# Performance work log

Measured on AMD Instinct MI355X. Metric: run time of the kernel, lower is better.

The kernel has to match this reference:

```python
import jax, jax.numpy as jnp
import numpy as np

N = 16384      # occupied voxels after upsample
M = 16384      # target (ground-truth) voxels
C = 64         # input feature channels
CU = 64        # upsampled feature channels
B = 4          # batch size (samples in sparse batch)
S = 64         # voxel grid span per axis
TARGET_POINTS_NUM = 8192   # points_num_list entry (kthvalue k)
DIST_UPPER_BOUND2 = 4.0    # dist_upper_bound ** 2


def _coord_key(c):
    # unique int64 key per (batch, x, y, z); all coords in [0, S)
    c = c.astype(jnp.int64)
    return ((c[:, 0] * S + c[:, 1]) * S + c[:, 2]) * S + c[:, 3]


def setup_inputs() -> dict:
    key = jax.random.key(0)
    k1, k2, k3, k4, k5, k6, k7 = jax.random.split(key, 7)
    fea = jax.random.normal(k1, (N, C), jnp.float32)
    coords = jnp.concatenate(
        [jax.random.randint(k2, (N, 1), 0, B, jnp.int32),
         jax.random.randint(k3, (N, 3), 0, S, jnp.int32)], axis=1)
    target_coords = jnp.concatenate(
        [jax.random.randint(k4, (M, 1), 0, B, jnp.int32),
         jax.random.randint(k5, (M, 3), 0, S, jnp.int32)], axis=1)
    W_up = jax.random.normal(k6, (C, CU), jnp.float32) / np.sqrt(C).astype(np.float32)
    W_cls = jax.random.normal(k7, (CU, 1), jnp.float32) / np.sqrt(CU).astype(np.float32)
    return {"fea": fea, "W_up": W_up, "W_cls": W_cls,
            "coords": coords, "target_coords": target_coords}


def reference(fea, W_up, W_cls, coords, target_coords):
    # upsample_block + classify_block (dense cores of the Minkowski blocks)
    fea_up = jax.nn.relu(fea @ W_up)              # [N, CU]
    pred = fea_up @ W_cls                          # [N, 1]
    p = pred[:, 0]

    # ---- keep mask ('Dist' loss: keep the TARGET_POINTS_NUM smallest) ----
    # torch.kthvalue(pred.F, k, dim=0): k-th smallest value
    thres = jnp.sort(p)[TARGET_POINTS_NUM - 1]
    keep = p <= thres                              # N > target_points_num branch

    # ---- get_target: keep_target via coordinate match (kernel_size=1 map) ----
    fk = _coord_key(coords)
    tk = jnp.sort(_coord_key(target_coords))
    idx = jnp.clip(jnp.searchsorted(tk, fk), 0, M - 1)
    keep_target = tk[idx] == fk                    # [N] bool

    # ---- get_target: per-sample K=1 KNN squared distances ----
    pc = coords[:, 1:].astype(jnp.float32)         # [N, 3]
    tc = target_coords[:, 1:].astype(jnp.float32)  # [M, 3]
    # |a-b|^2 = |a|^2 + |b|^2 - 2 a.b  (avoids [N,M,3] intermediate)
    d2 = (jnp.sum(pc * pc, -1)[:, None] + jnp.sum(tc * tc, -1)[None, :]
          - 2.0 * (pc @ tc.T))                     # [N, M]
    same_sample = coords[:, 0:1] == target_coords[None, :, 0]  # [N, M]
    d2 = jnp.where(same_sample, d2, jnp.inf)
    dists = jnp.maximum(jnp.min(d2, axis=1), 0.0)  # [N]

    # bound / ignore handling of loss_target
    pred_mask = p > DIST_UPPER_BOUND2
    target_mask = dists > DIST_UPPER_BOUND2
    loss_target = jnp.where(~pred_mask & target_mask, DIST_UPPER_BOUND2, dists)
    loss_target = jnp.where(pred_mask & target_mask, p, loss_target)

    keep = keep | keep_target
    # pruning: represented as masking (static shapes under jit)
    fea_pruned = fea_up * keep[:, None].astype(fea_up.dtype)
    return pred, fea_pruned, keep, keep_target, loss_target
```

## Files before the change

kernel.cpp:

```cpp
#include <hip/hip_runtime.h>
#include <math.h>

#define N_PTS 16384
#define M_TGT 16384
#define TPN 8192
#define DUB2 4.0f
#define BMASK_WORDS (4*64*64*64/32)
#define SCAT_NB 16

__device__ __forceinline__ unsigned int mono_key(float f) {
    unsigned int u = __float_as_uint(f);
    return (u & 0x80000000u) ? ~u : (u | 0x80000000u);
}

__device__ const signed char NOFF4[33][4] = {
    {0,0,0,0},
    {1,0,0,1},{-1,0,0,1},{0,1,0,1},{0,-1,0,1},{0,0,1,1},{0,0,-1,1},
    {1,1,0,2},{1,-1,0,2},{-1,1,0,2},{-1,-1,0,2},{1,0,1,2},{1,0,-1,2},{-1,0,1,2},{-1,0,-1,2},
    {0,1,1,2},{0,1,-1,2},{0,-1,1,2},{0,-1,-1,2},
    {1,1,1,3},{1,1,-1,3},{1,-1,1,3},{1,-1,-1,3},{-1,1,1,3},{-1,1,-1,3},{-1,-1,1,3},{-1,-1,-1,3},
    {2,0,0,4},{-2,0,0,4},{0,2,0,4},{0,-2,0,4},{0,0,2,4},{0,0,-2,4}
};

__device__ __forceinline__ void scan_locate256(const unsigned int* h256,
        unsigned int r, unsigned int* sh_b, unsigned int* sh_r, int tid) {
    const int lane = tid & 63;
    if ((tid >> 6) == 0) {
        uint4 h = ((const uint4*)h256)[lane];
        unsigned int ss = h.x + h.y + h.z + h.w;
        unsigned int inc = ss;
        for (int d = 1; d < 64; d <<= 1) {
            unsigned int t = __shfl_up(inc, d);
            if (lane >= d) inc += t;
        }
        unsigned int exc = inc - ss;
        bool has = (r >= exc && r < exc + ss);
        unsigned long long m = __ballot(has);
        if (m != 0ull && lane == __ffsll(m) - 1) {
            unsigned int rr = r - exc;
            if (rr < h.x)                   { *sh_b = lane*4u;    *sh_r = rr; }
            else if (rr < h.x+h.y)          { *sh_b = lane*4u+1u; *sh_r = rr-h.x; }
            else if (rr < h.x+h.y+h.z)      { *sh_b = lane*4u+2u; *sh_r = rr-h.x-h.y; }
            else                            { *sh_b = lane*4u+3u; *sh_r = rr-h.x-h.y-h.z; }
        }
    }
}

__global__ __launch_bounds__(256) void k_gemm(const float* __restrict__ fea,
        const float* __restrict__ Wup, const float* __restrict__ Wcls,
        float* __restrict__ out_pred, float* __restrict__ out_fea,
        unsigned int* __restrict__ bmask, unsigned int* __restrict__ hist16,
        unsigned int* __restrict__ phist) {
    __shared__ float Ws[64 * 64];
    __shared__ float fs[16 * 68];
    const int tid = threadIdx.x;
    const int r0 = blockIdx.x * 16;

    if (tid < 32) bmask[blockIdx.x * 32 + tid] = 0u;
    else if (tid < 96) hist16[blockIdx.x * 64 + tid - 32] = 0u;
    else if (tid < 100) phist[blockIdx.x * 4 + tid - 96] = 0u;

    for (int t = tid; t < 1024; t += 256)
        ((float4*)Ws)[t] = ((const float4*)Wup)[t];
    {
        float4 v = ((const float4*)(fea + r0 * 64))[tid];
        int r = tid >> 4, c = (tid & 15) * 4;
        fs[r*68 + c + 0] = v.x; fs[r*68 + c + 1] = v.y;
        fs[r*68 + c + 2] = v.z; fs[r*68 + c + 3] = v.w;
    }
    __syncthreads();

    const int cg = tid & 15;
    const int r  = tid >> 4;
    float a0 = 0.f, a1 = 0.f, a2 = 0.f, a3 = 0.f;
    const float* fr = fs + r * 68;
    #pragma unroll
    for (int k = 0; k < 64; ++k) {
        float f = fr[k];
        float4 w = *(const float4*)&Ws[k * 64 + cg * 4];
        a0 = fmaf(f, w.x, a0); a1 = fmaf(f, w.y, a1);
        a2 = fmaf(f, w.z, a2); a3 = fmaf(f, w.w, a3);
    }
    a0 = fmaxf(a0, 0.f); a1 = fmaxf(a1, 0.f);
    a2 = fmaxf(a2, 0.f); a3 = fmaxf(a3, 0.f);
    const int row = r0 + r;
    *(float4*)&out_fea[row * 64 + cg * 4] = make_float4(a0, a1, a2, a3);

    float4 wc = *(const float4*)&Wcls[cg * 4];
    float s = a0*wc.x + a1*wc.y + a2*wc.z + a3*wc.w;
    for (int off = 1; off < 16; off <<= 1) s += __shfl_xor(s, off, 16);
    if (cg == 0) out_pred[row] = s;
}

__global__ __launch_bounds__(256) void k_scat(const float* __restrict__ pred,
        const int* __restrict__ tc, unsigned int* __restrict__ bmask,
        unsigned int* __restrict__ phist, unsigned int* __restrict__ hist16) {
    __shared__ unsigned int whist[4][256];
    const int tid = threadIdx.x;
    const int blk = blockIdx.x;
    const int id = blk * 256 + tid;

    for (int t = tid; t < 4 * 256; t += 256) ((unsigned int*)whist)[t] = 0u;

    int4 c = *(const int4*)&tc[id * 4];
    int key = ((c.x * 64 + c.y) * 64 + c.z) * 64 + c.w;
    atomicOr(&bmask[key >> 5], 1u << (key & 31));

    __syncthreads();
    unsigned int u = mono_key(pred[id]);
    atomicAdd(&whist[tid >> 6][u >> 24], 1u);
    atomicAdd(&hist16[u >> 16], 1u);
    __syncthreads();
    {
        unsigned int s = whist[0][tid] + whist[1][tid] + whist[2][tid] + whist[3][tid];
        if (s) atomicAdd(&phist[(blk >> 2) * 256 + tid], s);
    }
}

__global__ __launch_bounds__(1024) void k_final(const int* __restrict__ coords,
        const unsigned int* __restrict__ bmask, const unsigned int* __restrict__ phist,
        const unsigned int* __restrict__ hist16,
        const float* __restrict__ out_pred, float* __restrict__ out_fea,
        float* __restrict__ out_keep, float* __restrict__ out_kt,
        float* __restrict__ out_loss) {
    __shared__ unsigned int hA[256];
    __shared__ unsigned int list[1024];
    __shared__ unsigned int sh_b, sh_r, sh_cnt;
    __shared__ float kscale[64];
    const int tid = threadIdx.x;
    const int r0 = blockIdx.x * 64;

    if (tid < 256) {
        unsigned int s = 0u;
        #pragma unroll
        for (int b = 0; b < SCAT_NB; ++b) s += phist[b * 256 + tid];
        hA[tid] = s;
    }
    if (tid == 0) sh_cnt = 0u;
    __syncthreads();
    scan_locate256(hA, TPN - 1, &sh_b, &sh_r, tid);
    __syncthreads();
    const unsigned int b0 = sh_b;
    const unsigned int rank1 = sh_r;

    if (tid < 256) hA[tid] = hist16[b0 * 256 + tid];
    __syncthreads();
    scan_locate256(hA, rank1, &sh_b, &sh_r, tid);
    __syncthreads();
    const unsigned int bin16 = (b0 << 8) | sh_b;
    const unsigned int rank2 = sh_r;

    for (int i = tid; i < N_PTS / 4; i += 1024) {
        float4 v = ((const float4*)out_pred)[i];
        unsigned int u0 = mono_key(v.x), u1 = mono_key(v.y);
        unsigned int u2 = mono_key(v.z), u3 = mono_key(v.w);
        if ((u0 >> 16) == bin16) { unsigned int p = atomicAdd(&sh_cnt, 1u); if (p < 1024u) list[p] = u0 & 0xFFFFu; }
        if ((u1 >> 16) == bin16) { unsigned int p = atomicAdd(&sh_cnt, 1u); if (p < 1024u) list[p] = u1 & 0xFFFFu; }
        if ((u2 >> 16) == bin16) { unsigned int p = atomicAdd(&sh_cnt, 1u); if (p < 1024u) list[p] = u2 & 0xFFFFu; }
        if ((u3 >> 16) == bin16) { unsigned int p = atomicAdd(&sh_cnt, 1u); if (p < 1024u) list[p] = u3 & 0xFFFFu; }
    }
    __syncthreads();
    const unsigned int cnt = sh_cnt;
    unsigned int b2, b3;

    if (cnt <= 1024u) {
        if (tid < 256) hA[tid] = 0u;
        __syncthreads();
        if (tid < (int)cnt) atomicAdd(&hA[list[tid] >> 8], 1u);
        __syncthreads();
        scan_locate256(hA, rank2, &sh_b, &sh_r, tid);
        __syncthreads();
        b2 = sh_b;
        unsigned int rank3 = sh_r;
        if (tid < 256) hA[tid] = 0u;
        __syncthreads();
        if (tid < (int)cnt) { unsigned int e = list[tid]; if ((e >> 8) == b2) atomicAdd(&hA[e & 255u], 1u); }
        __syncthreads();
        scan_locate256(hA, rank3, &sh_b, &sh_r, tid);
        __syncthreads();
        b3 = sh_b;
    } else {
        if (tid < 256) hA[tid] = 0u;
        __syncthreads();
        for (int i = tid; i < N_PTS / 4; i += 1024) {
            float4 v = ((const float4*)out_pred)[i];
            unsigned int u0 = mono_key(v.x), u1 = mono_key(v.y);
            unsigned int u2 = mono_key(v.z), u3 = mono_key(v.w);
            if ((u0 >> 16) == bin16) atomicAdd(&hA[(u0 >> 8) & 255u], 1u);
            if ((u1 >> 16) == bin16) atomicAdd(&hA[(u1 >> 8) & 255u], 1u);
            if ((u2 >> 16) == bin16) atomicAdd(&hA[(u2 >> 8) & 255u], 1u);
            if ((u3 >> 16) == bin16) atomicAdd(&hA[(u3 >> 8) & 255u], 1u);
        }
        __syncthreads();
        scan_locate256(hA, rank2, &sh_b, &sh_r, tid);
        __syncthreads();
        b2 = sh_b;
        unsigned int rank3 = sh_r;
        unsigned int pfx24 = (bin16 << 8) | b2;
        if (tid < 256) hA[tid] = 0u;
        __syncthreads();
        for (int i = tid; i < N_PTS / 4; i += 1024) {
            float4 v = ((const float4*)out_pred)[i];
            unsigned int u0 = mono_key(v.x), u1 = mono_key(v.y);
            unsigned int u2 = mono_key(v.z), u3 = mono_key(v.w);
            if ((u0 >> 8) == pfx24) atomicAdd(&hA[u0 & 255u], 1u);
            if ((u1 >> 8) == pfx24) atomicAdd(&hA[u1 & 255u], 1u);
            if ((u2 >> 8) == pfx24) atomicAdd(&hA[u2 & 255u], 1u);
            if ((u3 >> 8) == pfx24) atomicAdd(&hA[u3 & 255u], 1u);
        }
        __syncthreads();
        scan_locate256(hA, rank3, &sh_b, &sh_r, tid);
        __syncthreads();
        b3 = sh_b;
    }
    const unsigned int uth = (bin16 << 16) | (b2 << 8) | b3;
    const float thres = (uth & 0x80000000u) ? __uint_as_float(uth ^ 0x80000000u)
                                            : __uint_as_float(~uth);

    {
        const int row = tid >> 4;
        const int sub = tid & 15;
        const int i = r0 + row;
        float p = out_pred[i];
        int4 c = *(const int4*)&coords[i * 4];
        const int b = c.x, x = c.y, y = c.z, z = c.w;
        int key0 = ((b * 64 + x) * 64 + y) * 64 + z;
        bool kt = (bmask[key0 >> 5] >> (key0 & 31)) & 1u;
        float dists;
        if (kt) {
            dists = 0.f;
        } else {
            float best = 5.f;
            #pragma unroll
            for (int q = 0; q < 2; ++q) {
                int t = 1 + sub + q * 16;
                int ox = x + NOFF4[t][0], oy = y + NOFF4[t][1], oz = z + NOFF4[t][2];
                if (((unsigned)ox | (unsigned)oy | (unsigned)oz) < 64u) {
                    int key = ((b * 64 + ox) * 64 + oy) * 64 + oz;
                    if ((bmask[key >> 5] >> (key & 31)) & 1u)
                        best = fminf(best, (float)NOFF4[t][3]);
                }
            }
            for (int d = 1; d < 16; d <<= 1)
                best = fminf(best, __shfl_xor(best, d, 16));
            dists = best;
        }
        if (sub == 0) {
            bool keep0 = (p <= thres);
            bool pm = (p > DUB2), tm = (dists > DUB2);
            float loss = (pm && tm) ? p : ((!pm && tm) ? DUB2 : dists);
            bool kf = keep0 || kt;
            out_keep[i] = kf ? 1.f : 0.f;
            out_kt[i]  = kt ? 1.f : 0.f;
            out_loss[i] = loss;
            kscale[row] = kf ? 1.f : 0.f;
        }
    }
    __syncthreads();
    {
        float4* fbase = (float4*)(out_fea + r0 * 64);
        int v = tid;
        if (kscale[v >> 4] == 0.f)
            fbase[v] = make_float4(0.f, 0.f, 0.f, 0.f);
    }
}

extern "C" void kernel_launch(void* const* d_in, const int* in_sizes, int n_in,
                              void* d_out, int out_size, void* d_ws, size_t ws_size,
                              hipStream_t stream) {
    const float* fea     = (const float*)d_in[0];
    const float* Wup     = (const float*)d_in[1];
    const float* Wcls    = (const float*)d_in[2];
    const int*   coords  = (const int*)d_in[3];
    const int*   tcoords = (const int*)d_in[4];

    float* out      = (float*)d_out;
    float* out_pred = out;
    float* out_fea  = out + N_PTS;
    float* out_keep = out + N_PTS + N_PTS * 64;
    float* out_kt   = out_keep + N_PTS;
    float* out_loss = out_kt + N_PTS;

    char* ws = (char*)d_ws;
    unsigned int* bmask  = (unsigned int*)(ws + 64);
    unsigned int* hist16 = (unsigned int*)(ws + 131136);
    unsigned int* phist  = (unsigned int*)(ws + 393280);

    k_gemm <<<N_PTS / 16, 256, 0, stream>>>(fea, Wup, Wcls, out_pred, out_fea,
                                            bmask, hist16, phist);
    k_scat <<<64, 256, 0, stream>>>(out_pred, tcoords, bmask, phist, hist16);
    k_final<<<N_PTS / 64, 1024, 0, stream>>>(coords, bmask, phist, hist16,
                                             out_pred, out_fea, out_keep, out_kt, out_loss);
}
```

Before: 25.62 us.

## Fuse scatter and histogram into GEMM kernel, add separate zeroing kernel

The separate scatter kernel is removed. Target-coordinate bitmask marking and the pred radix histograms now happen inside the GEMM kernel, using global atomics directly on one 256-bin histogram instead of per-block partials. Workspace zeroing moves to a new small kernel launched first, so the launch count stays at three. This trades the scatter pass's extra read of pred for global atomic contention on hist16 and phist from every row.

```diff
diff --git a/kernel.cpp b/kernel.cpp
--- a/kernel.cpp
+++ b/kernel.cpp
@@ -5,8 +5,7 @@
 #define M_TGT 16384
 #define TPN 8192
 #define DUB2 4.0f
-#define BMASK_WORDS (4*64*64*64/32)
-#define SCAT_NB 16
+#define ZWORDS 98560
 
 __device__ __forceinline__ unsigned int mono_key(float f) {
     unsigned int u = __float_as_uint(f);
@@ -46,8 +45,14 @@
     }
 }
 
+__global__ __launch_bounds__(256) void k_zero(unsigned int* __restrict__ z) {
+    int i = blockIdx.x * 256 + threadIdx.x;
+    if (i < ZWORDS) z[i] = 0u;
+}
+
 __global__ __launch_bounds__(256) void k_gemm(const float* __restrict__ fea,
         const float* __restrict__ Wup, const float* __restrict__ Wcls,
+        const int* __restrict__ tcoords,
         float* __restrict__ out_pred, float* __restrict__ out_fea,
         unsigned int* __restrict__ bmask, unsigned int* __restrict__ hist16,
         unsigned int* __restrict__ phist) {
@@ -56,9 +61,11 @@
     const int tid = threadIdx.x;
     const int r0 = blockIdx.x * 16;
 
-    if (tid < 32) bmask[blockIdx.x * 32 + tid] = 0u;
-    else if (tid < 96) hist16[blockIdx.x * 64 + tid - 32] = 0u;
-    else if (tid < 100) phist[blockIdx.x * 4 + tid - 96] = 0u;
+    if (tid < 16) {
+        int4 c = *(const int4*)&tcoords[(blockIdx.x * 16 + tid) * 4];
+        int key = ((c.x * 64 + c.y) * 64 + c.z) * 64 + c.w;
+        atomicOr(&bmask[key >> 5], 1u << (key & 31));
+    }
 
     for (int t = tid; t < 1024; t += 256)
         ((float4*)Ws)[t] = ((const float4*)Wup)[t];
@@ -89,31 +96,11 @@
     float4 wc = *(const float4*)&Wcls[cg * 4];
     float s = a0*wc.x + a1*wc.y + a2*wc.z + a3*wc.w;
     for (int off = 1; off < 16; off <<= 1) s += __shfl_xor(s, off, 16);
-    if (cg == 0) out_pred[row] = s;
-}
-
-__global__ __launch_bounds__(256) void k_scat(const float* __restrict__ pred,
-        const int* __restrict__ tc, unsigned int* __restrict__ bmask,
-        unsigned int* __restrict__ phist, unsigned int* __restrict__ hist16) {
-    __shared__ unsigned int whist[4][256];
-    const int tid = threadIdx.x;
-    const int blk = blockIdx.x;
-    const int id = blk * 256 + tid;
-
-    for (int t = tid; t < 4 * 256; t += 256) ((unsigned int*)whist)[t] = 0u;
-
-    int4 c = *(const int4*)&tc[id * 4];
-    int key = ((c.x * 64 + c.y) * 64 + c.z) * 64 + c.w;
-    atomicOr(&bmask[key >> 5], 1u << (key & 31));
-
-    __syncthreads();
-    unsigned int u = mono_key(pred[id]);
-    atomicAdd(&whist[tid >> 6][u >> 24], 1u);
-    atomicAdd(&hist16[u >> 16], 1u);
-    __syncthreads();
-    {
-        unsigned int s = whist[0][tid] + whist[1][tid] + whist[2][tid] + whist[3][tid];
-        if (s) atomicAdd(&phist[(blk >> 2) * 256 + tid], s);
+    if (cg == 0) {
+        out_pred[row] = s;
+        unsigned int u = mono_key(s);
+        atomicAdd(&hist16[u >> 16], 1u);
+        atomicAdd(&phist[u >> 24], 1u);
     }
 }
 
@@ -130,12 +117,7 @@
     const int tid = threadIdx.x;
     const int r0 = blockIdx.x * 64;
 
-    if (tid < 256) {
-        unsigned int s = 0u;
-        #pragma unroll
-        for (int b = 0; b < SCAT_NB; ++b) s += phist[b * 256 + tid];
-        hA[tid] = s;
-    }
+    if (tid < 256) hA[tid] = phist[tid];
     if (tid == 0) sh_cnt = 0u;
     __syncthreads();
     scan_locate256(hA, TPN - 1, &sh_b, &sh_r, tid);
@@ -282,13 +264,14 @@
     float* out_loss = out_kt + N_PTS;
 
     char* ws = (char*)d_ws;
+    unsigned int* zbase  = (unsigned int*)(ws + 64);
     unsigned int* bmask  = (unsigned int*)(ws + 64);
     unsigned int* hist16 = (unsigned int*)(ws + 131136);
     unsigned int* phist  = (unsigned int*)(ws + 393280);
 
-    k_gemm <<<N_PTS / 16, 256, 0, stream>>>(fea, Wup, Wcls, out_pred, out_fea,
-                                            bmask, hist16, phist);
-    k_scat <<<64, 256, 0, stream>>>(out_pred, tcoords, bmask, phist, hist16);
+    k_zero <<<(ZWORDS + 255) / 256, 256, 0, stream>>>(zbase);
+    k_gemm <<<N_PTS / 16, 256, 0, stream>>>(fea, Wup, Wcls, tcoords,
+                                            out_pred, out_fea, bmask, hist16, phist);
     k_final<<<N_PTS / 64, 1024, 0, stream>>>(coords, bmask, phist, hist16,
                                              out_pred, out_fea, out_keep, out_kt, out_loss);
 }
```

New measurement: 94.99 us. 3.71x slower.
